# Kernel tuning notes

Hardware: AMD Instinct MI355X
Metric: run time of the kernel (lower is better)

Reference implementation:

```python
import jax, jax.numpy as jnp
import numpy as np

EMBED_DIM = 512
NUM_HEADS = 8
HEAD_DIM = EMBED_DIM // NUM_HEADS  # 64


def setup_inputs() -> dict:
    key = jax.random.key(0)
    ks = jax.random.split(key, 11)
    B, S, E, dh = 4, 2048, EMBED_DIM, HEAD_DIM
    s_small = 1.0 / np.sqrt(dh)
    s_big = 1.0 / np.sqrt(E)
    return {
        "Q": jax.random.normal(ks[0], (B, S, E), jnp.float32),
        "K": jax.random.normal(ks[1], (B, S, E), jnp.float32),
        "V": jax.random.normal(ks[2], (B, S, E), jnp.float32),
        "Wq_w": jax.random.normal(ks[3], (dh, dh), jnp.float32) * s_small,
        "Wq_b": jnp.zeros((dh,), jnp.float32),
        "Wk_w": jax.random.normal(ks[4], (dh, dh), jnp.float32) * s_small,
        "Wk_b": jnp.zeros((dh,), jnp.float32),
        "Wv_w": jax.random.normal(ks[5], (dh, dh), jnp.float32) * s_small,
        "Wv_b": jnp.zeros((dh,), jnp.float32),
        "Wo_w": jax.random.normal(ks[6], (E, E), jnp.float32) * s_big,
        "Wo_b": jnp.zeros((E,), jnp.float32),
    }


def reference(Q, K, V, Wq_w, Wq_b, Wk_w, Wk_b, Wv_w, Wv_b, Wo_w, Wo_b):
    B, S, E = Q.shape
    H, dh = NUM_HEADS, HEAD_DIM
    # split heads: [B,S,E] -> [B,S,H,dh]; per-head shared linear (torch y = x @ W.T + b)
    q = jnp.einsum('bshd,od->bsho', Q.reshape(B, S, H, dh), Wq_w) + Wq_b
    k = jnp.einsum('bshd,od->bsho', K.reshape(B, S, H, dh), Wk_w) + Wk_b
    v = jnp.einsum('bshd,od->bsho', V.reshape(B, S, H, dh), Wv_w) + Wv_b
    # [B,H,S,dh]
    q = q.transpose(0, 2, 1, 3)
    k = k.transpose(0, 2, 1, 3)
    v = v.transpose(0, 2, 1, 3)
    scores = jnp.einsum('bhqd,bhkd->bhqk', q, k) / np.sqrt(dh)  # full N x N scores (faithful to naive impl)
    probs = jax.nn.softmax(scores, axis=-1)
    attn = jnp.einsum('bhqk,bhkd->bhqd', probs, v)
    # combine heads: [B,H,S,dh] -> [B,S,E]
    out = attn.transpose(0, 2, 1, 3).reshape(B, S, E)
    return out @ Wo_w.T + Wo_b
```

## Files before the change

kernel.cpp:

```cpp
#include <hip/hip_runtime.h>

typedef float  f32x4  __attribute__((ext_vector_type(4)));
typedef float  f32x16 __attribute__((ext_vector_type(16)));
typedef short  s16x8  __attribute__((ext_vector_type(8)));

constexpr int Bn = 4, Sn = 2048, En = 512, Hn = 8;
constexpr int BH = Bn * Hn;
constexpr int NT = Sn / 64;
constexpr float QSCL = 0.125f * 1.44269504088896f;

static __device__ __forceinline__ ushort f2bf(float f) {
  union { float f; uint u; } v; v.f = f;
  uint r = v.u + 0x7fffu + ((v.u >> 16) & 1u);
  return (ushort)(r >> 16);
}
static __device__ __forceinline__ uint2 pack4(float a, float b, float c, float d) {
  union { ushort us[4]; uint2 u; } pk;
  pk.us[0] = f2bf(a); pk.us[1] = f2bf(b); pk.us[2] = f2bf(c); pk.us[3] = f2bf(d);
  return pk.u;
}
static __device__ __forceinline__ float hexp2(float x) {
  float r; asm("v_exp_f32 %0, %1" : "=v"(r) : "v"(x)); return r;
}
static __device__ __forceinline__ uint pkbf(float lo, float hi2) {
  uint r; asm("v_cvt_pk_bf16_f32 %0, %1, %2" : "=v"(r) : "v"(lo), "v"(hi2)); return r;
}
#define SWAP32(a, b) asm("v_permlane32_swap_b32 %0, %1" : "+v"(a), "+v"(b))
static __device__ __forceinline__ s16x8 mk8(uint a, uint b, uint c, uint d) {
  union { uint u[4]; s16x8 v; } x; x.u[0] = a; x.u[1] = b; x.u[2] = c; x.u[3] = d; return x.v;
}
#define MFMA32(A, B, C) __builtin_amdgcn_mfma_f32_32x32x16_bf16((A), (B), (C), 0, 0, 0)
#define GLDS(SRC, DST) __builtin_amdgcn_global_load_lds( \
    (const __attribute__((address_space(1))) void*)(SRC), \
    (__attribute__((address_space(3))) void*)(DST), 16, 0, 0)

__global__ __launch_bounds__(256) void proj_kernel(
    const float* __restrict__ Qi, const float* __restrict__ Ki, const float* __restrict__ Vi,
    const float* __restrict__ Wq, const float* __restrict__ bq,
    const float* __restrict__ Wk, const float* __restrict__ bk,
    const float* __restrict__ Wv, const float* __restrict__ bv,
    ushort* __restrict__ qo, ushort* __restrict__ ko, ushort* __restrict__ vto)
{
  constexpr int LP = 72;
  __shared__ ushort Xl[64 * LP];
  __shared__ ushort Wl[64 * LP];
  const int role = blockIdx.z;
  const float* X    = role == 0 ? Qi : (role == 1 ? Ki : Vi);
  const float* W    = role == 0 ? Wq : (role == 1 ? Wk : Wv);
  const float* bias = role == 0 ? bq : (role == 1 ? bk : bv);
  const float oscl  = role == 0 ? QSCL : 1.0f;
  const int t = threadIdx.x, lane = t & 63, w = t >> 6;
  const int g = lane >> 4, ql = lane & 15;
  const int bh = blockIdx.y, b = bh >> 3, h = bh & 7;
  const int s0 = blockIdx.x * 64;

  {
    const int row = t >> 4, c = t & 15;
#pragma unroll
    for (int p = 0; p < 4; ++p) {
      const int rr = row + p * 16;
      const float4 wv = *(const float4*)(W + rr * 64 + c * 4);
      *(uint2*)&Wl[rr * LP + c * 4] = pack4(wv.x, wv.y, wv.z, wv.w);
      const float4 xv = *(const float4*)(X + ((size_t)b * Sn + s0 + rr) * En + h * 64 + c * 4);
      *(uint2*)&Xl[rr * LP + c * 4] = pack4(xv.x, xv.y, xv.z, xv.w);
    }
  }
  __syncthreads();

  f32x4 acc[4];
#pragma unroll
  for (int i = 0; i < 4; ++i) acc[i] = (f32x4){0.f, 0.f, 0.f, 0.f};
#pragma unroll
  for (int kc = 0; kc < 2; ++kc) {
    const s16x8 bfrag = *(const s16x8*)&Xl[(w * 16 + ql) * LP + kc * 32 + g * 8];
#pragma unroll
    for (int nt = 0; nt < 4; ++nt) {
      const s16x8 afrag = *(const s16x8*)&Wl[(nt * 16 + ql) * LP + kc * 32 + g * 8];
      acc[nt] = __builtin_amdgcn_mfma_f32_16x16x32_bf16(afrag, bfrag, acc[nt], 0, 0, 0);
    }
  }

  const int s = s0 + w * 16 + ql;
  if (role < 2) {
    ushort* dst = (role == 0 ? qo : ko) + ((size_t)bh * Sn + s) * 64;
#pragma unroll
    for (int nt = 0; nt < 4; ++nt) {
      const int ob = nt * 16 + g * 4;
      *(uint2*)&dst[ob] = pack4((acc[nt][0] + bias[ob]) * oscl, (acc[nt][1] + bias[ob + 1]) * oscl,
                                (acc[nt][2] + bias[ob + 2]) * oscl, (acc[nt][3] + bias[ob + 3]) * oscl);
    }
  } else {
#pragma unroll
    for (int nt = 0; nt < 4; ++nt) {
#pragma unroll
      for (int r = 0; r < 4; ++r) {
        const int o = nt * 16 + g * 4 + r;
        vto[((size_t)bh * 64 + o) * Sn + s] = f2bf(acc[nt][r] + bias[o]);
      }
    }
  }
}

__global__ __launch_bounds__(512, 4) void flash_kernel(
    const ushort* __restrict__ q, const ushort* __restrict__ k,
    const ushort* __restrict__ vt, ushort* __restrict__ attn)
{
  __shared__ __align__(16) char smem[36864];
  float* mrg = (float*)smem;
  const int tid = threadIdx.x, lane = tid & 63, w = tid >> 6;
  const int m = lane & 31, hi = lane >> 5;
  const int wl = w & 3, h2 = w >> 2;
  const int hx  = hi ^ (m & 7);
  const int hxv = hx ^ (h2 << 2);

  int lid = blockIdx.x + (blockIdx.y << 4);
  lid = (lid & 7) * 64 + (lid >> 3);
  const int bq = lid & 15, bh = lid >> 4;
  const int qrow = bq * 128 + wl * 32 + m;
  const int b = bh >> 3, h = bh & 7;

  const ushort* qp = q + ((size_t)bh * Sn + qrow) * 64 + hi * 8;
  const s16x8 qf0 = *(const s16x8*)(qp + 0);
  const s16x8 qf1 = *(const s16x8*)(qp + 16);
  const s16x8 qf2 = *(const s16x8*)(qp + 32);
  const s16x8 qf3 = *(const s16x8*)(qp + 48);

  const int srow = tid >> 3, sc = tid & 7, scs = sc ^ (srow & 7);
  const ushort* kS = k  + (size_t)bh * Sn * 64 + (size_t)srow * 64 + scs * 8;
  const ushort* vS = vt + ((size_t)bh * 64 + srow) * Sn + scs * 8;
  const uint dO = (uint)(tid * 16);
  char* KB0 = smem;          char* KB1 = smem + 8192;
  char* VB0 = smem + 16384;  char* VB1 = smem + 24576;

  const f32x16 z16 = {};
  f32x16 acc0 = {}, acc1 = {}, asum = {};
  union { ushort us[8]; s16x8 v; } onesU;
#pragma unroll
  for (int i = 0; i < 8; ++i) onesU.us[i] = 0x3F80;
  const s16x8 ones = onesU.v;

  GLDS(kS, KB0 + dO); GLDS(vS, VB0 + dO);
  kS += 4096; vS += 64;

#define LDK(KB, S)     (*(const s16x8*)((KB)  + ((h2 * 32 + m) * 64 + (((2 * (S)) ^ hx ) << 3)) * 2))
#define LDV(VB, DT, S) (*(const s16x8*)((VB)  + (((DT) * 32 + m) * 64 + (((2 * (S)) ^ hxv) << 3)) * 2))

#define STEP(T, KB, VB, KBn, VBn) do {                                      \
    if ((T) < NT - 1) {                                                     \
      GLDS(kS, (KBn) + dO); GLDS(vS, (VBn) + dO);                           \
      kS += 4096; vS += 64;                                                 \
      asm volatile("s_waitcnt vmcnt(2)" ::: "memory");                      \
    } else {                                                                \
      asm volatile("s_waitcnt vmcnt(0)" ::: "memory");                      \
    }                                                                       \
    __builtin_amdgcn_s_barrier();                                           \
    __builtin_amdgcn_sched_barrier(0);                                      \
    f32x16 sta, stb;                                                        \
    __builtin_amdgcn_s_setprio(1);                                          \
    sta = MFMA32(LDK(KB, 0), qf0, z16);                                     \
    sta = MFMA32(LDK(KB, 1), qf1, sta);                                     \
    stb = MFMA32(LDK(KB, 2), qf2, z16);                                     \
    stb = MFMA32(LDK(KB, 3), qf3, stb);                                     \
    __builtin_amdgcn_s_setprio(0);                                          \
    f32x16 p;                                                               \
    _Pragma("unroll")                                                       \
    for (int i = 0; i < 16; ++i) p[i] = hexp2(sta[i] + stb[i]);             \
    uint uA, uB, uC, uD, uE, uF, uG, uH;                                    \
    uA = pkbf(p[0], p[1]);   uB = pkbf(p[4], p[5]);   SWAP32(uA, uB);       \
    uC = pkbf(p[2], p[3]);   uD = pkbf(p[6], p[7]);   SWAP32(uC, uD);       \
    uE = pkbf(p[8], p[9]);   uF = pkbf(p[12], p[13]); SWAP32(uE, uF);       \
    uG = pkbf(p[10], p[11]); uH = pkbf(p[14], p[15]); SWAP32(uG, uH);       \
    const s16x8 pb0 = mk8(uA, uC, uB, uD);                                  \
    const s16x8 pb1 = mk8(uE, uG, uF, uH);                                  \
    __builtin_amdgcn_s_setprio(1);                                          \
    acc0 = MFMA32(LDV(VB, 0, 0), pb0, acc0);                                \
    acc0 = MFMA32(LDV(VB, 0, 1), pb1, acc0);                                \
    acc1 = MFMA32(LDV(VB, 1, 0), pb0, acc1);                                \
    acc1 = MFMA32(LDV(VB, 1, 1), pb1, acc1);                                \
    asum = MFMA32(ones, pb0, asum);                                         \
    asum = MFMA32(ones, pb1, asum);                                         \
    __builtin_amdgcn_s_setprio(0);                                          \
    __builtin_amdgcn_s_barrier();                                           \
    __builtin_amdgcn_sched_barrier(0);                                      \
  } while (0)

  for (int T = 0; T < NT; T += 2) {
    STEP(T,     KB0, VB0, KB1, VB1);
    STEP(T + 1, KB1, VB1, KB0, VB0);
  }
#undef STEP
#undef LDK
#undef LDV

  const float lT = asum[0];
  float* mp = mrg + (size_t)(wl * 64 + lane) * 36;
  __syncthreads();
  if (h2) {
#pragma unroll
    for (int i = 0; i < 4; ++i) {
      f32x4 t0 = {acc0[4 * i], acc0[4 * i + 1], acc0[4 * i + 2], acc0[4 * i + 3]};
      f32x4 t1 = {acc1[4 * i], acc1[4 * i + 1], acc1[4 * i + 2], acc1[4 * i + 3]};
      *(f32x4*)(mp + 4 * i) = t0;
      *(f32x4*)(mp + 16 + 4 * i) = t1;
    }
    mp[32] = lT;
  }
  __syncthreads();
  if (!h2) {
    const float inv = 1.0f / (lT + mp[32]);
    ushort* ap = attn + ((size_t)(b * Sn + qrow)) * En + h * 64;
#pragma unroll
    for (int g2 = 0; g2 < 4; ++g2) {
      float a0 = (acc0[g2 * 4 + 0] + mp[g2 * 4 + 0]) * inv;
      float a1 = (acc0[g2 * 4 + 1] + mp[g2 * 4 + 1]) * inv;
      float a2 = (acc0[g2 * 4 + 2] + mp[g2 * 4 + 2]) * inv;
      float a3 = (acc0[g2 * 4 + 3] + mp[g2 * 4 + 3]) * inv;
      float c0 = (acc1[g2 * 4 + 0] + mp[16 + g2 * 4 + 0]) * inv;
      float c1 = (acc1[g2 * 4 + 1] + mp[16 + g2 * 4 + 1]) * inv;
      float c2 = (acc1[g2 * 4 + 2] + mp[16 + g2 * 4 + 2]) * inv;
      float c3 = (acc1[g2 * 4 + 3] + mp[16 + g2 * 4 + 3]) * inv;
      uint2 u0, u1;
      u0.x = pkbf(a0, a1); u0.y = pkbf(a2, a3);
      u1.x = pkbf(c0, c1); u1.y = pkbf(c2, c3);
      *(uint2*)&ap[g2 * 8 + hi * 4]      = u0;
      *(uint2*)&ap[32 + g2 * 8 + hi * 4] = u1;
    }
  }
}

__global__ __launch_bounds__(256) void outproj_kernel(
    const ushort* __restrict__ attn, const float* __restrict__ Wo,
    const float* __restrict__ bo, float* __restrict__ out)
{
  constexpr int LP = 72;
  __shared__ ushort Al[64 * LP];
  __shared__ ushort Wl[64 * LP];
  const int t = threadIdx.x, lane = t & 63, w = t >> 6;
  const int g = lane >> 4, ml = lane & 15;
  const int m0 = blockIdx.x * 64, n0 = blockIdx.y * 64;
  f32x4 acc[4];
#pragma unroll
  for (int i = 0; i < 4; ++i) acc[i] = (f32x4){0.f, 0.f, 0.f, 0.f};
  for (int e0 = 0; e0 < En; e0 += 64) {
    __syncthreads();
    {
      const int row = t >> 3, c = t & 7;
#pragma unroll
      for (int p = 0; p < 2; ++p) {
        const int rr = row + p * 32;
        const uint4 v = *(const uint4*)(attn + ((size_t)(m0 + rr)) * En + e0 + c * 8);
        *(uint4*)&Al[rr * LP + c * 8] = v;
      }
    }
    {
      const int row = t >> 4, c = t & 15;
#pragma unroll
      for (int p = 0; p < 4; ++p) {
        const int rr = row + p * 16;
        const float4 v = *(const float4*)(Wo + ((size_t)(n0 + rr)) * En + e0 + c * 4);
        *(uint2*)&Wl[rr * LP + c * 4] = pack4(v.x, v.y, v.z, v.w);
      }
    }
    __syncthreads();
#pragma unroll
    for (int kc = 0; kc < 2; ++kc) {
      const s16x8 bfrag = *(const s16x8*)&Al[(w * 16 + ml) * LP + kc * 32 + g * 8];
#pragma unroll
      for (int nt = 0; nt < 4; ++nt) {
        const s16x8 afrag = *(const s16x8*)&Wl[(nt * 16 + ml) * LP + kc * 32 + g * 8];
        acc[nt] = __builtin_amdgcn_mfma_f32_16x16x32_bf16(afrag, bfrag, acc[nt], 0, 0, 0);
      }
    }
  }
  const int mrow = m0 + w * 16 + ml;
#pragma unroll
  for (int nt = 0; nt < 4; ++nt) {
    const float4 bias = *(const float4*)(bo + n0 + nt * 16 + g * 4);
    float4 o;
    o.x = acc[nt][0] + bias.x;
    o.y = acc[nt][1] + bias.y;
    o.z = acc[nt][2] + bias.z;
    o.w = acc[nt][3] + bias.w;
    *(float4*)&out[(size_t)mrow * En + n0 + nt * 16 + g * 4] = o;
  }
}

extern "C" void kernel_launch(void* const* d_in, const int* in_sizes, int n_in,
                              void* d_out, int out_size, void* d_ws, size_t ws_size,
                              hipStream_t stream) {
  const float* Qi = (const float*)d_in[0];
  const float* Ki = (const float*)d_in[1];
  const float* Vi = (const float*)d_in[2];
  const float* Wq = (const float*)d_in[3];
  const float* bq = (const float*)d_in[4];
  const float* Wk = (const float*)d_in[5];
  const float* bk = (const float*)d_in[6];
  const float* Wv = (const float*)d_in[7];
  const float* bv = (const float*)d_in[8];
  const float* Wo = (const float*)d_in[9];
  const float* bo = (const float*)d_in[10];

  const size_t TEN = (size_t)BH * Sn * 64;
  ushort* qw  = (ushort*)d_ws;
  ushort* kw  = qw + TEN;
  ushort* vtw = kw + TEN;
  ushort* at  = vtw + TEN;

  proj_kernel<<<dim3(Sn / 64, BH, 3), 256, 0, stream>>>(
      Qi, Ki, Vi, Wq, bq, Wk, bk, Wv, bv, qw, kw, vtw);
  flash_kernel<<<dim3(16, 32), 512, 0, stream>>>(qw, kw, vtw, at);
  outproj_kernel<<<dim3(Bn * Sn / 64, En / 64), 256, 0, stream>>>(
      at, Wo, bo, (float*)d_out);
}
```

Baseline: 88.29 us.

## Software-pipeline QK and PV across tiles, replace ones-MFMA rowsum with VALU sum

Restructures the flash attention loop so each iteration issues the QK^T MFMAs for tile T alongside the PV MFMAs for tile T-1. The exp and pack of tile T can then overlap matrix-core work instead of serialising behind it. V now uses triple buffering, which grows LDS from 36 KB to 40 KB. The row sum of probabilities moves from two extra MFMAs against a ones vector to VALU adds plus a cross-half shuffle, trading matrix-core work for vector ALU work. The larger LDS footprint may lower occupancy at 4 blocks per CU, and the loop is no longer unrolled by two with fixed buffer pointers.

```diff
diff --git a/kernel.cpp b/kernel.cpp
--- a/kernel.cpp
+++ b/kernel.cpp
@@ -105,7 +105,7 @@
     const ushort* __restrict__ q, const ushort* __restrict__ k,
     const ushort* __restrict__ vt, ushort* __restrict__ attn)
 {
-  __shared__ __align__(16) char smem[36864];
+  __shared__ __align__(16) char smem[40960];
   float* mrg = (float*)smem;
   const int tid = threadIdx.x, lane = tid & 63, w = tid >> 6;
   const int m = lane & 31, hi = lane >> 5;
@@ -130,69 +130,97 @@
   const ushort* vS = vt + ((size_t)bh * 64 + srow) * Sn + scs * 8;
   const uint dO = (uint)(tid * 16);
   char* KB0 = smem;          char* KB1 = smem + 8192;
-  char* VB0 = smem + 16384;  char* VB1 = smem + 24576;
+  char* VB0 = smem + 16384;  char* VB1 = smem + 24576;  char* VB2 = smem + 32768;
 
   const f32x16 z16 = {};
-  f32x16 acc0 = {}, acc1 = {}, asum = {};
-  union { ushort us[8]; s16x8 v; } onesU;
-#pragma unroll
-  for (int i = 0; i < 8; ++i) onesU.us[i] = 0x3F80;
-  const s16x8 ones = onesU.v;
-
-  GLDS(kS, KB0 + dO); GLDS(vS, VB0 + dO);
-  kS += 4096; vS += 64;
-
-#define LDK(KB, S)     (*(const s16x8*)((KB)  + ((h2 * 32 + m) * 64 + (((2 * (S)) ^ hx ) << 3)) * 2))
-#define LDV(VB, DT, S) (*(const s16x8*)((VB)  + (((DT) * 32 + m) * 64 + (((2 * (S)) ^ hxv) << 3)) * 2))
-
-#define STEP(T, KB, VB, KBn, VBn) do {                                      \
-    if ((T) < NT - 1) {                                                     \
-      GLDS(kS, (KBn) + dO); GLDS(vS, (VBn) + dO);                           \
-      kS += 4096; vS += 64;                                                 \
-      asm volatile("s_waitcnt vmcnt(2)" ::: "memory");                      \
-    } else {                                                                \
-      asm volatile("s_waitcnt vmcnt(0)" ::: "memory");                      \
-    }                                                                       \
-    __builtin_amdgcn_s_barrier();                                           \
-    __builtin_amdgcn_sched_barrier(0);                                      \
-    f32x16 sta, stb;                                                        \
-    __builtin_amdgcn_s_setprio(1);                                          \
-    sta = MFMA32(LDK(KB, 0), qf0, z16);                                     \
-    sta = MFMA32(LDK(KB, 1), qf1, sta);                                     \
-    stb = MFMA32(LDK(KB, 2), qf2, z16);                                     \
-    stb = MFMA32(LDK(KB, 3), qf3, stb);                                     \
-    __builtin_amdgcn_s_setprio(0);                                          \
+  f32x16 acc0 = {}, acc1 = {};
+  float lsum = 0.f;
+  s16x8 pb0, pb1;
+
+#define LDK(KB, S)     (*(const s16x8*)((KB) + ((h2 * 32 + m) * 64 + (((2 * (S)) ^ hx ) << 3)) * 2))
+#define LDV(VB, DT, S) (*(const s16x8*)((VB) + (((DT) * 32 + m) * 64 + (((2 * (S)) ^ hxv) << 3)) * 2))
+
+#define SMPACK(STA, STB) do {                                               \
     f32x16 p;                                                               \
     _Pragma("unroll")                                                       \
-    for (int i = 0; i < 16; ++i) p[i] = hexp2(sta[i] + stb[i]);             \
+    for (int i = 0; i < 16; ++i) p[i] = hexp2((STA)[i] + (STB)[i]);         \
+    float s01 = (p[0] + p[1]) + (p[2] + p[3]);                              \
+    float s23 = (p[4] + p[5]) + (p[6] + p[7]);                              \
+    float s45 = (p[8] + p[9]) + (p[10] + p[11]);                            \
+    float s67 = (p[12] + p[13]) + (p[14] + p[15]);                          \
+    lsum += (s01 + s23) + (s45 + s67);                                      \
     uint uA, uB, uC, uD, uE, uF, uG, uH;                                    \
     uA = pkbf(p[0], p[1]);   uB = pkbf(p[4], p[5]);   SWAP32(uA, uB);       \
     uC = pkbf(p[2], p[3]);   uD = pkbf(p[6], p[7]);   SWAP32(uC, uD);       \
     uE = pkbf(p[8], p[9]);   uF = pkbf(p[12], p[13]); SWAP32(uE, uF);       \
     uG = pkbf(p[10], p[11]); uH = pkbf(p[14], p[15]); SWAP32(uG, uH);       \
-    const s16x8 pb0 = mk8(uA, uC, uB, uD);                                  \
-    const s16x8 pb1 = mk8(uE, uG, uF, uH);                                  \
-    __builtin_amdgcn_s_setprio(1);                                          \
-    acc0 = MFMA32(LDV(VB, 0, 0), pb0, acc0);                                \
-    acc0 = MFMA32(LDV(VB, 0, 1), pb1, acc0);                                \
-    acc1 = MFMA32(LDV(VB, 1, 0), pb0, acc1);                                \
-    acc1 = MFMA32(LDV(VB, 1, 1), pb1, acc1);                                \
-    asum = MFMA32(ones, pb0, asum);                                         \
-    asum = MFMA32(ones, pb1, asum);                                         \
-    __builtin_amdgcn_s_setprio(0);                                          \
-    __builtin_amdgcn_s_barrier();                                           \
-    __builtin_amdgcn_sched_barrier(0);                                      \
+    pb0 = mk8(uA, uC, uB, uD);                                              \
+    pb1 = mk8(uE, uG, uF, uH);                                              \
   } while (0)
 
-  for (int T = 0; T < NT; T += 2) {
-    STEP(T,     KB0, VB0, KB1, VB1);
-    STEP(T + 1, KB1, VB1, KB0, VB0);
-  }
-#undef STEP
+  GLDS(kS, KB0 + dO); GLDS(vS, VB0 + dO);
+  kS += 4096; vS += 64;
+
+  GLDS(kS, KB1 + dO); GLDS(vS, VB1 + dO);
+  kS += 4096; vS += 64;
+  asm volatile("s_waitcnt vmcnt(2)" ::: "memory");
+  __builtin_amdgcn_s_barrier();
+  __builtin_amdgcn_sched_barrier(0);
+  {
+    f32x16 sta, stb;
+    __builtin_amdgcn_s_setprio(1);
+    sta = MFMA32(LDK(KB0, 0), qf0, z16);
+    sta = MFMA32(LDK(KB0, 1), qf1, sta);
+    stb = MFMA32(LDK(KB0, 2), qf2, z16);
+    stb = MFMA32(LDK(KB0, 3), qf3, stb);
+    __builtin_amdgcn_s_setprio(0);
+    SMPACK(sta, stb);
+  }
+  __builtin_amdgcn_s_barrier();
+  __builtin_amdgcn_sched_barrier(0);
+
+  char *kcur = KB1, *knxt = KB0;
+  char *rPV = VB0, *rCUR = VB1, *rNXT = VB2;
+
+  for (int T = 1; T < NT; ++T) {
+    if (T < NT - 1) {
+      GLDS(kS, knxt + dO); GLDS(vS, rNXT + dO);
+      kS += 4096; vS += 64;
+      asm volatile("s_waitcnt vmcnt(2)" ::: "memory");
+    } else {
+      asm volatile("s_waitcnt vmcnt(0)" ::: "memory");
+    }
+    __builtin_amdgcn_s_barrier();
+    __builtin_amdgcn_sched_barrier(0);
+    f32x16 sta, stb;
+    __builtin_amdgcn_s_setprio(1);
+    sta = MFMA32(LDK(kcur, 0), qf0, z16);
+    sta = MFMA32(LDK(kcur, 1), qf1, sta);
+    stb = MFMA32(LDK(kcur, 2), qf2, z16);
+    stb = MFMA32(LDK(kcur, 3), qf3, stb);
+    acc0 = MFMA32(LDV(rPV, 0, 0), pb0, acc0);
+    acc0 = MFMA32(LDV(rPV, 0, 1), pb1, acc0);
+    acc1 = MFMA32(LDV(rPV, 1, 0), pb0, acc1);
+    acc1 = MFMA32(LDV(rPV, 1, 1), pb1, acc1);
+    __builtin_amdgcn_s_setprio(0);
+    SMPACK(sta, stb);
+    __builtin_amdgcn_s_barrier();
+    __builtin_amdgcn_sched_barrier(0);
+    { char* t0 = kcur; kcur = knxt; knxt = t0; }
+    { char* t1 = rPV; rPV = rCUR; rCUR = rNXT; rNXT = t1; }
+  }
+
+  __builtin_amdgcn_s_setprio(1);
+  acc0 = MFMA32(LDV(rPV, 0, 0), pb0, acc0);
+  acc0 = MFMA32(LDV(rPV, 0, 1), pb1, acc0);
+  acc1 = MFMA32(LDV(rPV, 1, 0), pb0, acc1);
+  acc1 = MFMA32(LDV(rPV, 1, 1), pb1, acc1);
+  __builtin_amdgcn_s_setprio(0);
 #undef LDK
 #undef LDV
-
-  const float lT = asum[0];
+#undef SMPACK
+
+  const float lT = lsum + __shfl_xor(lsum, 32);
   float* mp = mrg + (size_t)(wl * 64 + lane) * 36;
   __syncthreads();
   if (h2) {
```

After: 88.31 us. Within noise of the previous version (+0.0%).

## Enlarge outproj tiles to 128x128 with 512 threads; precompute flash LDS offsets

Applied to the files above, without the earlier changes.

The output projection now uses 128x128 tiles with 512 threads. Each wave computes a 64x32 sub-tile of 4x2 MFMA fragments, which raises register reuse of the A and B fragments and halves the number of blocks that re-read attn and Wo from global memory. In the flash kernel, the swizzled LDS byte offsets for K and V fragments are computed once before the loop instead of being rebuilt by the LDK/LDV macros each step, and the score sum is formed as a vector add before the exp. The larger tiles give fewer blocks (256) and raise LDS and register use per block, which may lower occupancy.

```diff
diff --git a/kernel.cpp b/kernel.cpp
--- a/kernel.cpp
+++ b/kernel.cpp
@@ -30,6 +30,7 @@
   union { uint u[4]; s16x8 v; } x; x.u[0] = a; x.u[1] = b; x.u[2] = c; x.u[3] = d; return x.v;
 }
 #define MFMA32(A, B, C) __builtin_amdgcn_mfma_f32_32x32x16_bf16((A), (B), (C), 0, 0, 0)
+#define MFMA16(A, B, C) __builtin_amdgcn_mfma_f32_16x16x32_bf16((A), (B), (C), 0, 0, 0)
 #define GLDS(SRC, DST) __builtin_amdgcn_global_load_lds( \
     (const __attribute__((address_space(1))) void*)(SRC), \
     (__attribute__((address_space(3))) void*)(DST), 16, 0, 0)
@@ -76,7 +77,7 @@
 #pragma unroll
     for (int nt = 0; nt < 4; ++nt) {
       const s16x8 afrag = *(const s16x8*)&Wl[(nt * 16 + ql) * LP + kc * 32 + g * 8];
-      acc[nt] = __builtin_amdgcn_mfma_f32_16x16x32_bf16(afrag, bfrag, acc[nt], 0, 0, 0);
+      acc[nt] = MFMA16(afrag, bfrag, acc[nt]);
     }
   }
 
@@ -113,6 +114,15 @@
   const int hx  = hi ^ (m & 7);
   const int hxv = hx ^ (h2 << 2);
 
+  const uint kof0 = (uint)((h2 * 32 + m) * 128 + (((0) ^ hx) << 4));
+  const uint kof1 = (uint)((h2 * 32 + m) * 128 + (((2) ^ hx) << 4));
+  const uint kof2 = (uint)((h2 * 32 + m) * 128 + (((4) ^ hx) << 4));
+  const uint kof3 = (uint)((h2 * 32 + m) * 128 + (((6) ^ hx) << 4));
+  const uint vof00 = (uint)((0 * 32 + m) * 128 + (((0) ^ hxv) << 4));
+  const uint vof01 = (uint)((0 * 32 + m) * 128 + (((2) ^ hxv) << 4));
+  const uint vof10 = (uint)((1 * 32 + m) * 128 + (((0) ^ hxv) << 4));
+  const uint vof11 = (uint)((1 * 32 + m) * 128 + (((2) ^ hxv) << 4));
+
   int lid = blockIdx.x + (blockIdx.y << 4);
   lid = (lid & 7) * 64 + (lid >> 3);
   const int bq = lid & 15, bh = lid >> 4;
@@ -141,9 +151,6 @@
 
   GLDS(kS, KB0 + dO); GLDS(vS, VB0 + dO);
   kS += 4096; vS += 64;
-
-#define LDK(KB, S)     (*(const s16x8*)((KB)  + ((h2 * 32 + m) * 64 + (((2 * (S)) ^ hx ) << 3)) * 2))
-#define LDV(VB, DT, S) (*(const s16x8*)((VB)  + (((DT) * 32 + m) * 64 + (((2 * (S)) ^ hxv) << 3)) * 2))
 
 #define STEP(T, KB, VB, KBn, VBn) do {                                      \
     if ((T) < NT - 1) {                                                     \
@@ -157,14 +164,15 @@
     __builtin_amdgcn_sched_barrier(0);                                      \
     f32x16 sta, stb;                                                        \
     __builtin_amdgcn_s_setprio(1);                                          \
-    sta = MFMA32(LDK(KB, 0), qf0, z16);                                     \
-    sta = MFMA32(LDK(KB, 1), qf1, sta);                                     \
-    stb = MFMA32(LDK(KB, 2), qf2, z16);                                     \
-    stb = MFMA32(LDK(KB, 3), qf3, stb);                                     \
+    sta = MFMA32(*(const s16x8*)((KB) + kof0), qf0, z16);                   \
+    sta = MFMA32(*(const s16x8*)((KB) + kof1), qf1, sta);                   \
+    stb = MFMA32(*(const s16x8*)((KB) + kof2), qf2, z16);                   \
+    stb = MFMA32(*(const s16x8*)((KB) + kof3), qf3, stb);                   \
     __builtin_amdgcn_s_setprio(0);                                          \
+    const f32x16 ss = sta + stb;                                            \
     f32x16 p;                                                               \
     _Pragma("unroll")                                                       \
-    for (int i = 0; i < 16; ++i) p[i] = hexp2(sta[i] + stb[i]);             \
+    for (int i = 0; i < 16; ++i) p[i] = hexp2(ss[i]);                       \
     uint uA, uB, uC, uD, uE, uF, uG, uH;                                    \
     uA = pkbf(p[0], p[1]);   uB = pkbf(p[4], p[5]);   SWAP32(uA, uB);       \
     uC = pkbf(p[2], p[3]);   uD = pkbf(p[6], p[7]);   SWAP32(uC, uD);       \
@@ -173,10 +181,10 @@
     const s16x8 pb0 = mk8(uA, uC, uB, uD);                                  \
     const s16x8 pb1 = mk8(uE, uG, uF, uH);                                  \
     __builtin_amdgcn_s_setprio(1);                                          \
-    acc0 = MFMA32(LDV(VB, 0, 0), pb0, acc0);                                \
-    acc0 = MFMA32(LDV(VB, 0, 1), pb1, acc0);                                \
-    acc1 = MFMA32(LDV(VB, 1, 0), pb0, acc1);                                \
-    acc1 = MFMA32(LDV(VB, 1, 1), pb1, acc1);                                \
+    acc0 = MFMA32(*(const s16x8*)((VB) + vof00), pb0, acc0);                \
+    acc0 = MFMA32(*(const s16x8*)((VB) + vof01), pb1, acc0);                \
+    acc1 = MFMA32(*(const s16x8*)((VB) + vof10), pb0, acc1);                \
+    acc1 = MFMA32(*(const s16x8*)((VB) + vof11), pb1, acc1);                \
     asum = MFMA32(ones, pb0, asum);                                         \
     asum = MFMA32(ones, pb1, asum);                                         \
     __builtin_amdgcn_s_setprio(0);                                          \
@@ -189,8 +197,6 @@
     STEP(T + 1, KB1, VB1, KB0, VB0);
   }
 #undef STEP
-#undef LDK
-#undef LDV
 
   const float lT = asum[0];
   float* mp = mrg + (size_t)(wl * 64 + lane) * 36;
@@ -228,60 +234,68 @@
   }
 }
 
-__global__ __launch_bounds__(256) void outproj_kernel(
+__global__ __launch_bounds__(512) void outproj_kernel(
     const ushort* __restrict__ attn, const float* __restrict__ Wo,
     const float* __restrict__ bo, float* __restrict__ out)
 {
   constexpr int LP = 72;
-  __shared__ ushort Al[64 * LP];
-  __shared__ ushort Wl[64 * LP];
+  __shared__ ushort Al[128 * LP];
+  __shared__ ushort Wl[128 * LP];
   const int t = threadIdx.x, lane = t & 63, w = t >> 6;
   const int g = lane >> 4, ml = lane & 15;
-  const int m0 = blockIdx.x * 64, n0 = blockIdx.y * 64;
-  f32x4 acc[4];
-#pragma unroll
-  for (int i = 0; i < 4; ++i) acc[i] = (f32x4){0.f, 0.f, 0.f, 0.f};
+  const int wm = w >> 2, wn = w & 3;
+  const int m0 = blockIdx.x * 128, n0 = blockIdx.y * 128;
+  f32x4 acc[4][2];
+#pragma unroll
+  for (int i = 0; i < 4; ++i)
+#pragma unroll
+    for (int j = 0; j < 2; ++j) acc[i][j] = (f32x4){0.f, 0.f, 0.f, 0.f};
+
+  const int srow = t >> 2, c0 = t & 3;
   for (int e0 = 0; e0 < En; e0 += 64) {
     __syncthreads();
-    {
-      const int row = t >> 3, c = t & 7;
-#pragma unroll
-      for (int p = 0; p < 2; ++p) {
-        const int rr = row + p * 32;
-        const uint4 v = *(const uint4*)(attn + ((size_t)(m0 + rr)) * En + e0 + c * 8);
-        *(uint4*)&Al[rr * LP + c * 8] = v;
+#pragma unroll
+    for (int p = 0; p < 2; ++p) {
+      const int c = c0 + p * 4;
+      const uint4 v = *(const uint4*)(attn + ((size_t)(m0 + srow)) * En + e0 + c * 8);
+      *(uint4*)&Al[srow * LP + c * 8] = v;
+    }
+#pragma unroll
+    for (int p = 0; p < 4; ++p) {
+      const int c = c0 + p * 4;
+      const float4 v = *(const float4*)(Wo + ((size_t)(n0 + srow)) * En + e0 + c * 4);
+      *(uint2*)&Wl[srow * LP + c * 4] = pack4(v.x, v.y, v.z, v.w);
+    }
+    __syncthreads();
+#pragma unroll
+    for (int kc = 0; kc < 2; ++kc) {
+      s16x8 bfr[4];
+#pragma unroll
+      for (int mf = 0; mf < 4; ++mf)
+        bfr[mf] = *(const s16x8*)&Al[(wm * 64 + mf * 16 + ml) * LP + kc * 32 + g * 8];
+#pragma unroll
+      for (int nf = 0; nf < 2; ++nf) {
+        const s16x8 afr = *(const s16x8*)&Wl[(wn * 32 + nf * 16 + ml) * LP + kc * 32 + g * 8];
+#pragma unroll
+        for (int mf = 0; mf < 4; ++mf)
+          acc[mf][nf] = MFMA16(afr, bfr[mf], acc[mf][nf]);
       }
     }
-    {
-      const int row = t >> 4, c = t & 15;
-#pragma unroll
-      for (int p = 0; p < 4; ++p) {
-        const int rr = row + p * 16;
-        const float4 v = *(const float4*)(Wo + ((size_t)(n0 + rr)) * En + e0 + c * 4);
-        *(uint2*)&Wl[rr * LP + c * 4] = pack4(v.x, v.y, v.z, v.w);
-      }
-    }
-    __syncthreads();
-#pragma unroll
-    for (int kc = 0; kc < 2; ++kc) {
-      const s16x8 bfrag = *(const s16x8*)&Al[(w * 16 + ml) * LP + kc * 32 + g * 8];
-#pragma unroll
-      for (int nt = 0; nt < 4; ++nt) {
-        const s16x8 afrag = *(const s16x8*)&Wl[(nt * 16 + ml) * LP + kc * 32 + g * 8];
-        acc[nt] = __builtin_amdgcn_mfma_f32_16x16x32_bf16(afrag, bfrag, acc[nt], 0, 0, 0);
-      }
-    }
-  }
-  const int mrow = m0 + w * 16 + ml;
-#pragma unroll
-  for (int nt = 0; nt < 4; ++nt) {
-    const float4 bias = *(const float4*)(bo + n0 + nt * 16 + g * 4);
-    float4 o;
-    o.x = acc[nt][0] + bias.x;
-    o.y = acc[nt][1] + bias.y;
-    o.z = acc[nt][2] + bias.z;
-    o.w = acc[nt][3] + bias.w;
-    *(float4*)&out[(size_t)mrow * En + n0 + nt * 16 + g * 4] = o;
+  }
+#pragma unroll
+  for (int mf = 0; mf < 4; ++mf) {
+    const int mrow = m0 + wm * 64 + mf * 16 + ml;
+#pragma unroll
+    for (int nf = 0; nf < 2; ++nf) {
+      const int ncol = n0 + wn * 32 + nf * 16 + g * 4;
+      const float4 bias = *(const float4*)(bo + ncol);
+      float4 o;
+      o.x = acc[mf][nf][0] + bias.x;
+      o.y = acc[mf][nf][1] + bias.y;
+      o.z = acc[mf][nf][2] + bias.z;
+      o.w = acc[mf][nf][3] + bias.w;
+      *(float4*)&out[(size_t)mrow * En + ncol] = o;
+    }
   }
 }
 
@@ -309,6 +323,6 @@
   proj_kernel<<<dim3(Sn / 64, BH, 3), 256, 0, stream>>>(
       Qi, Ki, Vi, Wq, bq, Wk, bk, Wv, bv, qw, kw, vtw);
   flash_kernel<<<dim3(16, 32), 512, 0, stream>>>(qw, kw, vtw, at);
-  outproj_kernel<<<dim3(Bn * Sn / 64, En / 64), 256, 0, stream>>>(
+  outproj_kernel<<<dim3(Bn * Sn / 128, En / 128), 512, 0, stream>>>(
       at, Wo, bo, (float*)d_out);
 }
```

New measurement: 86.41 us. -2.1%, faster.
